# Kernel optimization log

Measured on AMD Instinct MI355X. Metric: run time of the kernel, lower is better.

Reference implementation:

```python
import jax, jax.numpy as jnp
import numpy as np
import math

BLOCK_SIZE = 64
GATE_HIDDEN = 128


def _rmsnorm(x, w, eps=1e-6):
    v = jnp.mean(jnp.square(x), axis=-1, keepdims=True)
    return x * jax.lax.rsqrt(v + eps) * w


def _rotate_half(x):
    x1, x2 = jnp.split(x, 2, axis=-1)
    return jnp.concatenate([-x2, x1], axis=-1)


def _rope(x, cos, sin):
    # x: [B, S, H, D]; cos/sin: [B, S, D] -> unsqueeze head dim (unsqueeze_dim=2)
    c = cos[:, :, None, :]
    s = sin[:, :, None, :]
    return x * c + _rotate_half(x) * s


def setup_inputs() -> dict:
    key = jax.random.key(0)
    ks = jax.random.split(key, 10)
    B, S, Hk, D = 4, 65536, 8, 128
    Hq, g, Dg = 32, 4, GATE_HIDDEN
    nb = S // BLOCK_SIZE
    xav_q = math.sqrt(6.0 / (D + Dg))
    xav_k = math.sqrt(6.0 / (2 * D + Dg))
    return {
        "k": jax.random.normal(ks[0], (B, S, Hk, D), jnp.float32),
        "q": jax.random.normal(ks[1], (B, 1, Hq, D), jnp.float32),
        "Wq": jax.random.uniform(ks[2], (Hk, g, D, Dg), jnp.float32, -xav_q, xav_q),
        "Wk": jax.random.uniform(ks[3], (Hk, 2 * D, Dg), jnp.float32, -xav_k, xav_k),
        "qnorm_w": jnp.ones((Dg,), jnp.float32),
        "knorm_w": jnp.ones((Dg,), jnp.float32),
        "cos_q": jax.random.uniform(ks[4], (B, 1, Dg), jnp.float32, -1.0, 1.0),
        "sin_q": jax.random.uniform(ks[5], (B, 1, Dg), jnp.float32, -1.0, 1.0),
        "cos_k": jax.random.uniform(ks[6], (B, nb, Dg), jnp.float32, -1.0, 1.0),
        "sin_k": jax.random.uniform(ks[7], (B, nb, Dg), jnp.float32, -1.0, 1.0),
        "attention_mask": jnp.ones((B, Hk, nb), jnp.bool_),
        "block_budget": 128,
    }


def reference(k, q, Wq, Wk, qnorm_w, knorm_w, cos_q, sin_q, cos_k, sin_k,
              attention_mask, block_budget):
    B, S, Hk, D = k.shape
    nb = S // BLOCK_SIZE
    g = q.shape[2] // Hk
    Dg = Wk.shape[-1]
    scale = 1.0 / math.sqrt(Dg)

    # --- K path: block pooling (avg + max) -> per-head linear -> RMSNorm -> RoPE
    kb = k.reshape(B, nb, BLOCK_SIZE, Hk, D)
    k_pooled = jnp.concatenate([kb.mean(axis=2), kb.max(axis=2)], axis=-1)  # [B,nb,Hk,2D]
    k_c = jnp.einsum('bshi,hio->bsho', k_pooled, Wk)                         # [B,nb,Hk,Dg]
    k_c = _rmsnorm(k_c, knorm_w)
    k_c = _rope(k_c, cos_k, sin_k)

    # --- Q path (Qproj): grouped per-k-head projection -> RMSNorm -> RoPE
    qg = q.reshape(B, 1, Hk, g, D)
    qp = jnp.einsum('bskgi,kgio->bsko', qg, Wq)                              # [B,1,Hk,Dg]
    qp = _rmsnorm(qp, qnorm_w)
    qp = _rope(qp, cos_q, sin_q)
    qv = qp[:, 0]                                                            # [B,Hk,Dg]

    # --- gate scores + softmax
    attn = jnp.einsum('bhd,bshd->bhs', qv, k_c) * scale                      # [B,Hk,nb]
    attn = jnp.where(attention_mask, attn, jnp.float32(-1e20))
    attn = jax.nn.softmax(attn, axis=-1)

    # --- token_budget sparse block mask: topk + scatter
    _, topk_idx = jax.lax.top_k(attn, block_budget)                          # [B,Hk,k]
    blk = jnp.arange(nb)
    mask = jnp.any(topk_idx[..., :, None] == blk[None, None, None, :], axis=-2)
    mask = mask & attention_mask
    mask = mask.at[:, :, -1].set(True)
    return mask
```

## Files before the change

kernel.cpp:

```cpp
#include <hip/hip_runtime.h>
#include <hip/hip_bf16.h>
#include <math.h>

#define NB   1024
#define HKH  8

typedef float f4 __attribute__((ext_vector_type(4)));

__global__ __launch_bounds__(512) void qproj_kernel(const float* __restrict__ q,
                                                    const float* __restrict__ Wq,
                                                    const float* __restrict__ qnw,
                                                    const float* __restrict__ cq,
                                                    const float* __restrict__ sq,
                                                    float* __restrict__ qv) {
    int b = blockIdx.x >> 3, h = blockIdx.x & 7;
    int t = threadIdx.x;
    int o = t & 127, seg = t >> 7;
    __shared__ float qs[512];
    __shared__ float part[4][128];
    __shared__ float red[2];
    __shared__ float ybuf[128];
    qs[t] = q[(size_t)b * 4096 + (size_t)h * 512 + t];
    __syncthreads();
    const float* wqp = Wq + (size_t)h * 512 * 128 + o;
    float acc = 0.0f;
    int g0 = seg * 128;
#pragma unroll 4
    for (int gi = g0; gi < g0 + 128; ++gi)
        acc = fmaf(qs[gi], wqp[(size_t)gi * 128], acc);
    part[seg][o] = acc;
    __syncthreads();
    if (t < 128) {
        float a = part[0][o] + part[1][o] + part[2][o] + part[3][o];
        ybuf[o] = a;
        float ss = a * a;
        for (int off = 32; off > 0; off >>= 1) ss += __shfl_xor(ss, off);
        if ((o & 63) == 0) red[o >> 6] = ss;
    }
    __syncthreads();
    if (t < 128) {
        float scale = rsqrtf((red[0] + red[1]) * (1.0f / 128.0f) + 1e-6f);
        float y  = ybuf[o] * scale * qnw[o];
        int op   = (o < 64) ? o + 64 : o - 64;
        float yp = ybuf[op] * scale * qnw[op];
        float rot = (o < 64) ? -yp : yp;
        qv[((size_t)b * HKH + h) * 128 + o] =
            fmaf(y, cq[b * 128 + o], rot * sq[b * 128 + o]);
    }
}

__global__ __launch_bounds__(256) void fused_kernel(const float* __restrict__ kin,
                                                    const float* __restrict__ Wk,
                                                    const float* __restrict__ knw,
                                                    const float* __restrict__ cosk,
                                                    const float* __restrict__ sink,
                                                    const float* __restrict__ qv,
                                                    float* __restrict__ scores) {
    __shared__ float At[32][256];
    int wg   = blockIdx.x;
    int h    = wg & 7;
    int tile = (wg >> 3) & 31;
    int b    = wg >> 8;
    int t    = threadIdx.x;

    {
        int tc = t & 31;
        int tr = t >> 5;
        const float inv = 1.0f / 64.0f;
#pragma unroll
        for (int bi = 0; bi < 4; ++bi) {
            int blk = tr * 4 + bi;
            size_t row0 = (size_t)b * 65536 + ((size_t)tile * 32 + blk) * 64;
            const f4* src = (const f4*)(kin + row0 * 1024 + (size_t)h * 128) + tc;
            f4 v = __builtin_nontemporal_load(src);
            f4 s = v, m = v;
#pragma unroll 8
            for (int r = 1; r < 64; ++r) {
                f4 u = __builtin_nontemporal_load(src + (size_t)r * 256);
                s += u;
                m.x = fmaxf(m.x, u.x); m.y = fmaxf(m.y, u.y);
                m.z = fmaxf(m.z, u.z); m.w = fmaxf(m.w, u.w);
            }
            int sw = blk & 7;
            f4 mean = { s.x * inv, s.y * inv, s.z * inv, s.w * inv };
            *(f4*)&At[blk][(tc ^ sw) << 2]        = mean;
            *(f4*)&At[blk][((tc + 32) ^ sw) << 2] = m;
        }
    }
    __syncthreads();

    int cg = t & 15;
    int rg = t >> 4;
    int r0 = rg * 2, r1 = r0 + 1;
    int s0 = r0 & 7, s1 = r1 & 7;
    float acc0[8], acc1[8];
#pragma unroll
    for (int j = 0; j < 8; ++j) { acc0[j] = 0.0f; acc1[j] = 0.0f; }
    const float* Wb = Wk + (size_t)h * 256 * 128 + cg * 8;
#pragma unroll 2
    for (int kq = 0; kq < 64; ++kq) {
        f4 a0 = *(const f4*)&At[r0][(kq ^ s0) << 2];
        f4 a1 = *(const f4*)&At[r1][(kq ^ s1) << 2];
        const float* wrow = Wb + (size_t)kq * 512;
#pragma unroll
        for (int dk = 0; dk < 4; ++dk) {
            f4 w0 = *(const f4*)(wrow + dk * 128);
            f4 w1 = *(const f4*)(wrow + dk * 128 + 4);
            float av0 = a0[dk], av1 = a1[dk];
            acc0[0] = fmaf(av0, w0.x, acc0[0]); acc0[1] = fmaf(av0, w0.y, acc0[1]);
            acc0[2] = fmaf(av0, w0.z, acc0[2]); acc0[3] = fmaf(av0, w0.w, acc0[3]);
            acc0[4] = fmaf(av0, w1.x, acc0[4]); acc0[5] = fmaf(av0, w1.y, acc0[5]);
            acc0[6] = fmaf(av0, w1.z, acc0[6]); acc0[7] = fmaf(av0, w1.w, acc0[7]);
            acc1[0] = fmaf(av1, w0.x, acc1[0]); acc1[1] = fmaf(av1, w0.y, acc1[1]);
            acc1[2] = fmaf(av1, w0.z, acc1[2]); acc1[3] = fmaf(av1, w0.w, acc1[3]);
            acc1[4] = fmaf(av1, w1.x, acc1[4]); acc1[5] = fmaf(av1, w1.y, acc1[5]);
            acc1[6] = fmaf(av1, w1.z, acc1[6]); acc1[7] = fmaf(av1, w1.w, acc1[7]);
        }
    }

    float kn[8], qvr[8];
    const float* qvp = qv + ((size_t)b * HKH + h) * 128 + cg * 8;
#pragma unroll
    for (int j = 0; j < 8; ++j) { kn[j] = knw[cg * 8 + j]; qvr[j] = qvp[j]; }
#pragma unroll
    for (int i = 0; i < 2; ++i) {
        float* acc = i ? acc1 : acc0;
        int blkg = tile * 32 + r0 + i;
        float ss = 0.0f;
#pragma unroll
        for (int j = 0; j < 8; ++j) ss = fmaf(acc[j], acc[j], ss);
#pragma unroll
        for (int off = 1; off < 16; off <<= 1) ss += __shfl_xor(ss, off);
        float scale = rsqrtf(ss * (1.0f / 128.0f) + 1e-6f);
        const float* cb = cosk + ((size_t)b * NB + blkg) * 128 + cg * 8;
        const float* sb = sink + ((size_t)b * NB + blkg) * 128 + cg * 8;
        float part = 0.0f;
#pragma unroll
        for (int j = 0; j < 8; ++j) {
            float y  = acc[j] * scale * kn[j];
            float yp = __shfl_xor(y, 8);
            float rot = (cg < 8) ? -yp : yp;
            float z = fmaf(y, cb[j], rot * sb[j]);
            part = fmaf(z, qvr[j], part);
        }
#pragma unroll
        for (int off = 1; off < 16; off <<= 1) part += __shfl_xor(part, off);
        if (cg == 0)
            scores[((size_t)b * HKH + h) * NB + blkg] = part * 0.08838834764831845f;
    }
}

__device__ inline bool read_mask(const void* amp, int mode, size_t idx) {
    if (mode == 1) return ((const int*)amp)[idx] != 0;
    if (mode == 2) return ((const unsigned int*)amp)[idx] != 0u;
    return ((const unsigned char*)amp)[idx] != 0;
}

__global__ __launch_bounds__(512) void topk_kernel(const float* __restrict__ scores,
                                                   const void* __restrict__ amraw,
                                                   const int* __restrict__ bbp,
                                                   int* __restrict__ out) {
    int b = blockIdx.x >> 3, h = blockIdx.x & 7;
    int t = threadIdx.x;
    __shared__ float sv[NB];
    __shared__ int mode_sh;

    if (t == 0) {
        const unsigned int* w = (const unsigned int*)amraw;
        bool allint = true, allflt = true;
        for (int i = 0; i < 64; ++i) {
            unsigned int x = w[i];
            if (x != 0u && x != 1u) allint = false;
            if (x != 0u && x != 0x3f800000u) allflt = false;
        }
        mode_sh = allint ? 1 : (allflt ? 2 : 0);
    }
    __syncthreads();
    int mode = mode_sh;
    size_t rowoff = ((size_t)b * HKH + h) * NB;
    const float* src = scores + rowoff;
    for (int s = t; s < NB; s += 512)
        sv[s] = read_mask(amraw, mode, rowoff + s) ? src[s] : -1e20f;
    __syncthreads();

    int bb = bbp[0];
    if (bb > NB) bb = NB;
    if (bb < 1)  bb = 1;

    int e0 = t, e1 = t + 512;
    float v0 = sv[e0], v1 = sv[e1];
    int r0 = 0, r1 = 0;
#pragma unroll 4
    for (int j4 = 0; j4 < 256; ++j4) {
        f4 w = *(const f4*)&sv[j4 * 4];
        int jb = j4 * 4;
        r0 += (w.x > v0) + (w.y > v0) + (w.z > v0) + (w.w > v0);
        r1 += (w.x > v1) + (w.y > v1) + (w.z > v1) + (w.w > v1);
        r0 += (w.x == v0 && jb + 0 < e0) + (w.y == v0 && jb + 1 < e0)
            + (w.z == v0 && jb + 2 < e0) + (w.w == v0 && jb + 3 < e0);
        r1 += (w.x == v1 && jb + 0 < e1) + (w.y == v1 && jb + 1 < e1)
            + (w.z == v1 && jb + 2 < e1) + (w.w == v1 && jb + 3 < e1);
    }
    int* dst = out + rowoff;
    bool am0 = read_mask(amraw, mode, rowoff + e0);
    bool am1 = read_mask(amraw, mode, rowoff + e1);
    dst[e0] = ((r0 < bb && am0)) ? 1 : 0;
    dst[e1] = ((r1 < bb && am1) || (e1 == NB - 1)) ? 1 : 0;
}

extern "C" void kernel_launch(void* const* d_in, const int* in_sizes, int n_in,
                              void* d_out, int out_size, void* d_ws, size_t ws_size,
                              hipStream_t stream) {
    (void)in_sizes; (void)n_in; (void)out_size; (void)ws_size;
    const float* k   = (const float*)d_in[0];
    const float* q   = (const float*)d_in[1];
    const float* Wq  = (const float*)d_in[2];
    const float* Wk  = (const float*)d_in[3];
    const float* qnw = (const float*)d_in[4];
    const float* knw = (const float*)d_in[5];
    const float* cq  = (const float*)d_in[6];
    const float* sq  = (const float*)d_in[7];
    const float* ck  = (const float*)d_in[8];
    const float* sk  = (const float*)d_in[9];
    const void*  am  = d_in[10];
    const int*   bb  = (const int*)d_in[11];
    int* out = (int*)d_out;

    float* qv     = (float*)d_ws;
    float* scores = qv + 4 * HKH * 128;

    qproj_kernel<<<32, 512, 0, stream>>>(q, Wq, qnw, cq, sq, qv);
    fused_kernel<<<1024, 256, 0, stream>>>(k, Wk, knw, ck, sk, qv, scores);
    topk_kernel<<<32, 512, 0, stream>>>(scores, am, bb, out);
}
```

Baseline: 285.7 us.

## Remap fused kernel so each workgroup covers all heads for four blocks

Each workgroup now processes 4 consecutive K blocks across all 8 heads instead of 32 blocks for one head. Every load therefore reads a full 4KB token row contiguously, where before it read a 512B per-head slice. The shared-memory tile is transposed and swizzled so each head-warp runs a 256-deep dot product with 4x4 register accumulators, and the reductions now span 32 lanes. This makes the dominant streaming read more coalesced. The cost is that the Wk reuse per workgroup drops from 32 blocks to 4 and there is more per-element shared-memory scatter.

```diff
diff --git a/kernel.cpp b/kernel.cpp
--- a/kernel.cpp
+++ b/kernel.cpp
@@ -56,22 +56,20 @@
                                                     const float* __restrict__ sink,
                                                     const float* __restrict__ qv,
                                                     float* __restrict__ scores) {
-    __shared__ float At[32][256];
+    __shared__ float At[256][32];
     int wg   = blockIdx.x;
-    int h    = wg & 7;
-    int tile = (wg >> 3) & 31;
+    int tile = wg & 255;
     int b    = wg >> 8;
     int t    = threadIdx.x;
+    int h    = t >> 5;
+    int c    = t & 31;
 
     {
-        int tc = t & 31;
-        int tr = t >> 5;
         const float inv = 1.0f / 64.0f;
 #pragma unroll
         for (int bi = 0; bi < 4; ++bi) {
-            int blk = tr * 4 + bi;
-            size_t row0 = (size_t)b * 65536 + ((size_t)tile * 32 + blk) * 64;
-            const f4* src = (const f4*)(kin + row0 * 1024 + (size_t)h * 128) + tc;
+            size_t row0 = (size_t)b * 65536 + (size_t)tile * 256 + (size_t)bi * 64;
+            const f4* src = (const f4*)kin + row0 * 256 + t;
             f4 v = __builtin_nontemporal_load(src);
             f4 s = v, m = v;
 #pragma unroll 8
@@ -81,71 +79,62 @@
                 m.x = fmaxf(m.x, u.x); m.y = fmaxf(m.y, u.y);
                 m.z = fmaxf(m.z, u.z); m.w = fmaxf(m.w, u.w);
             }
-            int sw = blk & 7;
-            f4 mean = { s.x * inv, s.y * inv, s.z * inv, s.w * inv };
-            *(f4*)&At[blk][(tc ^ sw) << 2]        = mean;
-            *(f4*)&At[blk][((tc + 32) ^ sw) << 2] = m;
-        }
-    }
-    __syncthreads();
-
-    int cg = t & 15;
-    int rg = t >> 4;
-    int r0 = rg * 2, r1 = r0 + 1;
-    int s0 = r0 & 7, s1 = r1 & 7;
-    float acc0[8], acc1[8];
-#pragma unroll
-    for (int j = 0; j < 8; ++j) { acc0[j] = 0.0f; acc1[j] = 0.0f; }
-    const float* Wb = Wk + (size_t)h * 256 * 128 + cg * 8;
-#pragma unroll 2
-    for (int kq = 0; kq < 64; ++kq) {
-        f4 a0 = *(const f4*)&At[r0][(kq ^ s0) << 2];
-        f4 a1 = *(const f4*)&At[r1][(kq ^ s1) << 2];
-        const float* wrow = Wb + (size_t)kq * 512;
-#pragma unroll
-        for (int dk = 0; dk < 4; ++dk) {
-            f4 w0 = *(const f4*)(wrow + dk * 128);
-            f4 w1 = *(const f4*)(wrow + dk * 128 + 4);
-            float av0 = a0[dk], av1 = a1[dk];
-            acc0[0] = fmaf(av0, w0.x, acc0[0]); acc0[1] = fmaf(av0, w0.y, acc0[1]);
-            acc0[2] = fmaf(av0, w0.z, acc0[2]); acc0[3] = fmaf(av0, w0.w, acc0[3]);
-            acc0[4] = fmaf(av0, w1.x, acc0[4]); acc0[5] = fmaf(av0, w1.y, acc0[5]);
-            acc0[6] = fmaf(av0, w1.z, acc0[6]); acc0[7] = fmaf(av0, w1.w, acc0[7]);
-            acc1[0] = fmaf(av1, w0.x, acc1[0]); acc1[1] = fmaf(av1, w0.y, acc1[1]);
-            acc1[2] = fmaf(av1, w0.z, acc1[2]); acc1[3] = fmaf(av1, w0.w, acc1[3]);
-            acc1[4] = fmaf(av1, w1.x, acc1[4]); acc1[5] = fmaf(av1, w1.y, acc1[5]);
-            acc1[6] = fmaf(av1, w1.z, acc1[6]); acc1[7] = fmaf(av1, w1.w, acc1[7]);
-        }
-    }
-
-    float kn[8], qvr[8];
-    const float* qvp = qv + ((size_t)b * HKH + h) * 128 + cg * 8;
-#pragma unroll
-    for (int j = 0; j < 8; ++j) { kn[j] = knw[cg * 8 + j]; qvr[j] = qvp[j]; }
-#pragma unroll
-    for (int i = 0; i < 2; ++i) {
-        float* acc = i ? acc1 : acc0;
-        int blkg = tile * 32 + r0 + i;
+#pragma unroll
+            for (int j = 0; j < 4; ++j) {
+                int k0 = c * 4 + j;
+                int g  = (k0 >> 3) & 7;
+                At[k0      ][((h ^ g) << 2) | bi] = s[j] * inv;
+                At[k0 + 128][((h ^ g) << 2) | bi] = m[j];
+            }
+        }
+    }
+    __syncthreads();
+
+    float acc[4][4];
+#pragma unroll
+    for (int i = 0; i < 4; ++i)
+#pragma unroll
+        for (int j = 0; j < 4; ++j) acc[i][j] = 0.0f;
+    const float* wp = Wk + (size_t)h * 32768 + c * 4;
+#pragma unroll 4
+    for (int k = 0; k < 256; ++k) {
+        int g = (k >> 3) & 7;
+        f4 a = *(const f4*)&At[k][(h ^ g) << 2];
+        f4 w = *(const f4*)(wp + (size_t)k * 128);
+#pragma unroll
+        for (int i = 0; i < 4; ++i) {
+            acc[i][0] = fmaf(a[i], w.x, acc[i][0]);
+            acc[i][1] = fmaf(a[i], w.y, acc[i][1]);
+            acc[i][2] = fmaf(a[i], w.z, acc[i][2]);
+            acc[i][3] = fmaf(a[i], w.w, acc[i][3]);
+        }
+    }
+
+    f4 kn  = *(const f4*)(knw + c * 4);
+    f4 qvr = *(const f4*)(qv + ((size_t)b * HKH + h) * 128 + c * 4);
+#pragma unroll
+    for (int i = 0; i < 4; ++i) {
+        int blkg = tile * 4 + i;
         float ss = 0.0f;
 #pragma unroll
-        for (int j = 0; j < 8; ++j) ss = fmaf(acc[j], acc[j], ss);
-#pragma unroll
-        for (int off = 1; off < 16; off <<= 1) ss += __shfl_xor(ss, off);
+        for (int j = 0; j < 4; ++j) ss = fmaf(acc[i][j], acc[i][j], ss);
+#pragma unroll
+        for (int off = 1; off < 32; off <<= 1) ss += __shfl_xor(ss, off);
         float scale = rsqrtf(ss * (1.0f / 128.0f) + 1e-6f);
-        const float* cb = cosk + ((size_t)b * NB + blkg) * 128 + cg * 8;
-        const float* sb = sink + ((size_t)b * NB + blkg) * 128 + cg * 8;
+        f4 cb = *(const f4*)(cosk + ((size_t)b * NB + blkg) * 128 + c * 4);
+        f4 sb = *(const f4*)(sink + ((size_t)b * NB + blkg) * 128 + c * 4);
         float part = 0.0f;
 #pragma unroll
-        for (int j = 0; j < 8; ++j) {
-            float y  = acc[j] * scale * kn[j];
-            float yp = __shfl_xor(y, 8);
-            float rot = (cg < 8) ? -yp : yp;
+        for (int j = 0; j < 4; ++j) {
+            float y  = acc[i][j] * scale * kn[j];
+            float yp = __shfl_xor(y, 16);
+            float rot = (c < 16) ? -yp : yp;
             float z = fmaf(y, cb[j], rot * sb[j]);
             part = fmaf(z, qvr[j], part);
         }
 #pragma unroll
-        for (int off = 1; off < 16; off <<= 1) part += __shfl_xor(part, off);
-        if (cg == 0)
+        for (int off = 1; off < 32; off <<= 1) part += __shfl_xor(part, off);
+        if (c == 0)
             scores[((size_t)b * HKH + h) * NB + blkg] = part * 0.08838834764831845f;
     }
 }
```

Measured after the change: 258.1 us. 9.7% less time.
